# Kernel tuning notes

Hardware: AMD Instinct MI355X
Metric: run time of the kernel (lower is better)

Reference implementation:

```python
import jax, jax.numpy as jnp
import numpy as np

B, LQ, LKV, LT, C, H = 4, 1024, 1344, 320, 768, 12
DH = C // H
SCALE = DH ** -0.5
HID = 4 * C
EPS = 1e-5


def _ln(x, g, b):
    m = jnp.mean(x, axis=-1, keepdims=True)
    v = jnp.mean((x - m) ** 2, axis=-1, keepdims=True)
    return (x - m) * jax.lax.rsqrt(v + EPS) * g + b


def setup_inputs() -> dict:
    key = jax.random.key(0)
    ks = jax.random.split(key, 16)
    s = lambda k, shape, sc=0.02: jax.random.normal(k, shape, dtype=jnp.float32) * sc
    return {
        "tem_mask": s(ks[0], (B, LT, C), 1.0),
        "q": s(ks[1], (B, LQ, C), 1.0),
        "kv": s(ks[2], (B, LKV, C), 1.0),
        "attn_pos": s(ks[3], (1, H, LQ, LKV), 1.0),
        "ln1q_g": jnp.ones((C,)), "ln1q_b": jnp.zeros((C,)),
        "ln1kv_g": jnp.ones((C,)), "ln1kv_b": jnp.zeros((C,)),
        "Wq": s(ks[4], (C, C)), "bq": jnp.zeros((C,)),
        "Wkv": s(ks[5], (C, 2 * C)), "bkv": jnp.zeros((2 * C,)),
        "Wp": s(ks[6], (C, C)), "bp": jnp.zeros((C,)),
        "ln2_g": jnp.ones((C,)), "ln2_b": jnp.zeros((C,)),
        "W1": s(ks[7], (C, HID)), "b1": jnp.zeros((HID,)),
        "W2": s(ks[8], (HID, C)), "b2": jnp.zeros((C,)),
    }


def reference(tem_mask, q, kv, attn_pos, ln1q_g, ln1q_b, ln1kv_g, ln1kv_b,
              Wq, bq, Wkv, bkv, Wp, bp, ln2_g, ln2_b, W1, b1, W2, b2):
    qn = _ln(q, ln1q_g, ln1q_b)
    kvn = _ln(kv, ln1kv_g, ln1kv_b)
    # projections (attn_pos_encoding_only branch)
    qh = (qn @ Wq + bq).reshape(B, LQ, H, DH).transpose(0, 2, 1, 3)  # (B,H,Lq,Dh)
    kvp = kvn @ Wkv + bkv
    k, v = kvp[:, :, :C], kvp[:, :, C:]
    v = v.at[:, :LT, :].add(tem_mask)  # add template mask to template tokens
    kh = k.reshape(B, LKV, H, DH).transpose(0, 2, 1, 3)
    vh = v.reshape(B, LKV, H, DH).transpose(0, 2, 1, 3)
    attn = jnp.einsum('bhqd,bhkd->bhqk', qh, kh) * SCALE + attn_pos
    attn = jax.nn.softmax(attn, axis=-1)
    x = jnp.einsum('bhqk,bhkd->bhqd', attn, vh)
    x = x.transpose(0, 2, 1, 3).reshape(B, LQ, C)
    x = x @ Wp + bp
    q = q + x  # residual 1 (drop_path = Identity, dropout eval)
    h = _ln(q, ln2_g, ln2_b)
    h = jax.nn.gelu(h @ W1 + b1, approximate=False)
    h = h @ W2 + b2
    return q + h
```

## Files before the change

kernel.cpp:

```cpp
#include <hip/hip_runtime.h>
#include <hip/hip_bf16.h>
#include <math.h>

typedef __bf16 bf16x8 __attribute__((ext_vector_type(8)));
typedef float f32x4 __attribute__((ext_vector_type(4)));

__device__ __forceinline__ __hip_bfloat16 f2bf(float v){ return __float2bfloat16(v); }

__device__ __forceinline__ void gload16(const void* g, void* l){
  __builtin_amdgcn_global_load_lds(
      (const __attribute__((address_space(1))) void*)g,
      (__attribute__((address_space(3))) void*)l, 16, 0, 0);
}

__device__ __forceinline__ void ln_body(const float* rp, const float* g, const float* b,
                                        __hip_bfloat16* op, int t){
  float x0 = rp[t], x1 = rp[t+256], x2 = rp[t+512];
  float s = x0+x1+x2, ss = x0*x0+x1*x1+x2*x2;
#pragma unroll
  for(int o=32;o>0;o>>=1){ s += __shfl_down(s,o); ss += __shfl_down(ss,o); }
  __shared__ float red[10];
  if((t&63)==0){ red[t>>6]=s; red[4+(t>>6)]=ss; }
  __syncthreads();
  if(t==0){
    float S=red[0]+red[1]+red[2]+red[3], SS=red[4]+red[5]+red[6]+red[7];
    float m=S*(1.f/768.f);
    red[8]=m; red[9]=SS*(1.f/768.f)-m*m;
  }
  __syncthreads();
  float m=red[8], r=rsqrtf(red[9]+1e-5f);
  op[t]     = f2bf((x0-m)*r*g[t]     + b[t]);
  op[t+256] = f2bf((x1-m)*r*g[t+256] + b[t+256]);
  op[t+512] = f2bf((x2-m)*r*g[t+512] + b[t+512]);
}

__global__ __launch_bounds__(256) void prep_kernel(
    const float* __restrict__ Wq, const float* __restrict__ Wkv,
    const float* __restrict__ Wp, const float* __restrict__ W1,
    const float* __restrict__ W2,
    __hip_bfloat16* __restrict__ oq, __hip_bfloat16* __restrict__ okv,
    __hip_bfloat16* __restrict__ op_, __hip_bfloat16* __restrict__ o1,
    __hip_bfloat16* __restrict__ o2,
    const float* __restrict__ q, const float* __restrict__ kv,
    const float* __restrict__ qg, const float* __restrict__ qb,
    const float* __restrict__ kg, const float* __restrict__ kb2,
    __hip_bfloat16* __restrict__ qn, __hip_bfloat16* __restrict__ kvn){
  const int bid = blockIdx.x;
  const int tid = threadIdx.x;
  if(bid < 6912){
    __shared__ float tile[32][33];
    const float* in; __hip_bfloat16* out; int K, N, local;
    if(bid < 576)        { in=Wq;  out=oq;  K=768;  N=768;  local=bid; }
    else if(bid < 1728)  { in=Wkv; out=okv; K=768;  N=1536; local=bid-576; }
    else if(bid < 2304)  { in=Wp;  out=op_; K=768;  N=768;  local=bid-1728; }
    else if(bid < 4608)  { in=W1;  out=o1;  K=768;  N=3072; local=bid-2304; }
    else                 { in=W2;  out=o2;  K=3072; N=768;  local=bid-4608; }
    const int nbx = N/32;
    const int n0 = (local % nbx)*32, k0 = (local / nbx)*32;
    const int tx = tid & 31, ty = tid >> 5;
#pragma unroll
    for(int i=0;i<4;i++) tile[ty+i*8][tx] = in[(size_t)(k0+ty+i*8)*N + n0+tx];
    __syncthreads();
#pragma unroll
    for(int i=0;i<4;i++) out[(size_t)(n0+ty+i*8)*K + k0+tx] = f2bf(tile[tx][ty+i*8]);
  } else {
    int row = bid - 6912;
    if(row < 4096) ln_body(q + (size_t)row*768, qg, qb, qn + (size_t)row*768, tid);
    else { row -= 4096; ln_body(kv + (size_t)row*768, kg, kb2, kvn + (size_t)row*768, tid); }
  }
}

__global__ __launch_bounds__(256) void ln_kernel(const float* __restrict__ in,
    const float* __restrict__ g, const float* __restrict__ b,
    __hip_bfloat16* __restrict__ out){
  int row = blockIdx.x, t = threadIdx.x;
  ln_body(in + (size_t)row*768, g, b, out + (size_t)row*768, t);
}

template<int BM, int BN, int EPI>
__global__ __launch_bounds__(256) void gemm_gl(
    const __hip_bfloat16* __restrict__ A, const __hip_bfloat16* __restrict__ BT,
    const float* __restrict__ bias, int M, int N, int K,
    void* __restrict__ out, const void* __restrict__ aux0, void* __restrict__ out2){
  constexpr int WR = (BM==128 || BN==64) ? 2 : 1;
  constexpr int WC = 4/WR;
  constexpr int MF = BM/(WR*16);
  constexpr int NF = BN/(WC*16);
  constexpr int NBUF = (BM==64 && BN==64) ? 3 : 2;
  constexpr int LPS = BM/32 + BN/32;
  __shared__ char sA[NBUF][BM*128];
  __shared__ char sB[NBUF][BN*128];
  const int tid = threadIdx.x;
  const int l = tid & 63, w = tid >> 6;
  const int lg = l >> 4, li = l & 15;
  const int wrow = (WR==2) ? (w>>1)*(BM/2) : 0;
  const int wcol = (WC==2) ? (w&1)*(BN/2) : w*(BN/4);
  const int bm = blockIdx.x * BM;
  const int bn = blockIdx.y * BN;
  const int arow = w*(BM/4) + (l>>3);
  const int brow = w*(BN/4) + (l>>3);
  const int scol = ((((l&7)*16) ^ ((l>>3)<<4)) >> 1);

  auto stage = [&](int buf, int kt){
    const int k0 = kt*64;
#pragma unroll
    for(int i=0;i<BM/32;i++)
      gload16(A  + (size_t)(bm+arow+i*8)*K + k0 + scol, sA[buf] + (w*(BM/4))*128 + i*1024);
#pragma unroll
    for(int i=0;i<BN/32;i++)
      gload16(BT + (size_t)(bn+brow+i*8)*K + k0 + scol, sB[buf] + (w*(BN/4))*128 + i*1024);
  };

  f32x4 acc[MF][NF] = {};
  const int nk = K >> 6;

  if constexpr(NBUF==3){
    stage(0, 0);
    stage(1, 1);
  } else {
    stage(0, 0);
    __syncthreads();
  }

  for(int kt=0; kt<nk; ++kt){
    const char *cA, *cB;
    if constexpr(NBUF==3){
      if(kt+1 < nk) asm volatile("s_waitcnt vmcnt(%0)" :: "i"(LPS) : "memory");
      else          asm volatile("s_waitcnt vmcnt(0)" ::: "memory");
      __builtin_amdgcn_s_barrier();
      if(kt+2 < nk) stage((kt+2)%3, kt+2);
      cA = sA[kt%3]; cB = sB[kt%3];
    } else {
      const int cur = kt & 1;
      if(kt+1 < nk) stage(cur^1, kt+1);
      cA = sA[cur]; cB = sB[cur];
    }
#pragma unroll
    for(int kk=0;kk<2;kk++){
      const int kb = kk*64 + lg*16;
      bf16x8 af[MF], bfr[NF];
#pragma unroll
      for(int m=0;m<MF;m++){
        int row = wrow+m*16+li;
        af[m] = *(const bf16x8*)(cA + row*128 + (kb ^ ((row&7)<<4)));
      }
#pragma unroll
      for(int n=0;n<NF;n++){
        int row = wcol+n*16+li;
        bfr[n] = *(const bf16x8*)(cB + row*128 + (kb ^ ((row&7)<<4)));
      }
#pragma unroll
      for(int m=0;m<MF;m++)
#pragma unroll
        for(int n=0;n<NF;n++)
          acc[m][n] = __builtin_amdgcn_mfma_f32_16x16x32_bf16(af[m], bfr[n], acc[m][n],0,0,0);
    }
    if constexpr(NBUF==2) __syncthreads();
  }
#pragma unroll
  for(int m=0;m<MF;m++){
#pragma unroll
    for(int n=0;n<NF;n++){
      if constexpr(EPI==1){
        const int col = bn + wcol + n*16 + li;
        const int row0 = bm + wrow + m*16 + lg*4;
        const int bb = row0 / 1344, ii = row0 % 1344;
        if(col < 768){
#pragma unroll
          for(int r=0;r<4;r++)
            ((__hip_bfloat16*)out)[(size_t)(row0+r)*768 + col] = f2bf(acc[m][n][r] + bias[col]);
        } else {
          const int c = col - 768, hh = c >> 6, d = c & 63;
          __hip_bfloat16 tmp[4];
#pragma unroll
          for(int r=0;r<4;r++){
            float v = acc[m][n][r] + bias[col];
            if(ii < 320) v += ((const float*)aux0)[((size_t)bb*320 + ii + r)*768 + c];
            tmp[r] = f2bf(v);
          }
          *(uint2*)((__hip_bfloat16*)out2 + ((size_t)(bb*12+hh)*64 + d)*1344 + ii) = *(const uint2*)tmp;
        }
      } else {
#pragma unroll
        for(int r=0;r<4;r++){
          int row = bm + wrow + m*16 + lg*4 + r;
          int col = bn + wcol + n*16 + li;
          float v = acc[m][n][r] + bias[col];
          if constexpr(EPI==0){
            ((__hip_bfloat16*)out)[(size_t)row*N + col] = f2bf(v * 0.125f);
          } else if constexpr(EPI==2){
            v += ((const float*)aux0)[(size_t)row*N + col];
            ((float*)out)[(size_t)row*N + col] = v;
          } else if constexpr(EPI==3){
            float u = v*(0.7978845608f + 0.0356774081f*v*v);
            float e = __expf(-2.f*fabsf(u));
            float th = (1.f - e)/(1.f + e);
            th = (u < 0.f) ? -th : th;
            ((__hip_bfloat16*)out)[(size_t)row*N + col] = f2bf(0.5f*v*(1.f+th));
          } else {
            v += ((const float*)aux0)[(size_t)row*N + col];
            ((float*)out)[(size_t)row*N + col] = v;
          }
        }
      }
    }
  }
}

__global__ __launch_bounds__(256) void attn_kernel(
    const __hip_bfloat16* __restrict__ qh,
    const __hip_bfloat16* __restrict__ kb,
    const __hip_bfloat16* __restrict__ vt,
    const float* __restrict__ pos,
    __hip_bfloat16* __restrict__ xo){
  __shared__ char sK[2][8192];
  __shared__ char sV[2][8192];
  __shared__ char sP[4][2048];
  const int bid = blockIdx.x;
  const int qt = bid & 15, h = (bid >> 4) % 12, b = bid / 192;
  const int q0 = qt * 64;
  const int tid = threadIdx.x;
  const int l = tid & 63, w = tid >> 6;
  const int lg = l >> 4, li = l & 15;

  const int srow = w*16 + (l>>3);
  const int soff = (((l&7)*16) ^ ((l>>3)<<4)) >> 1;
  const __hip_bfloat16* ksrc = kb + ((size_t)b*1344 + srow)*768 + h*64 + soff;
  const __hip_bfloat16* vsrc = vt + ((size_t)(b*12+h)*64 + srow)*1344 + soff;

  bf16x8 aq[2];
  {
    const char* qp = (const char*)(qh + ((size_t)(b*1024 + q0 + w*16 + li))*768 + h*64);
    aq[0] = *(const bf16x8*)(qp + lg*16);
    aq[1] = *(const bf16x8*)(qp + 64 + lg*16);
  }
  bf16x8 ones;
#pragma unroll
  for(int i=0;i<8;i++) ones[i] = (__bf16)1.0f;
  const size_t posbase = ((size_t)h*1024 + q0 + w*16 + lg*4)*1344 + li;

  f32x4 accO[4] = {};
  f32x4 accL = {};
  float mrun[4];
#pragma unroll
  for(int r=0;r<4;r++) mrun[r] = -1e30f;

  auto stage = [&](int buf, int t){
    const size_t ko = (size_t)t*64*768;
    const size_t vo = (size_t)t*64;
    gload16(ksrc + ko,          sK[buf] + w*2048);
    gload16(ksrc + ko + 8*768,  sK[buf] + w*2048 + 1024);
    gload16(vsrc + vo,          sV[buf] + w*2048);
    gload16(vsrc + vo + 8*1344, sV[buf] + w*2048 + 1024);
  };
  auto ldpos = [&](int t, float (&pr)[4][4]){
    const float* pp = pos + posbase + (size_t)t*64;
#pragma unroll
    for(int n=0;n<4;n++)
#pragma unroll
      for(int r=0;r<4;r++)
        pr[n][r] = __builtin_nontemporal_load(pp + (size_t)r*1344 + n*16);
  };

  float pA[4][4], pB[4][4];
  ldpos(0, pA);
  stage(0, 0);
  __syncthreads();

  char* sPw = sP[w];

  auto body = [&](int t, float (&posr)[4][4], float (&npos)[4][4]){
    const int cur = t & 1;
    const bool more = (t < 20);
    f32x4 accS[4] = {};
    __builtin_amdgcn_s_setprio(1);
#pragma unroll
    for(int kk=0; kk<2; ++kk){
      const int kbyte = kk*64 + lg*16;
#pragma unroll
      for(int n=0;n<4;n++){
        int row = n*16 + li;
        bf16x8 bkf = *(const bf16x8*)(sK[cur] + row*128 + (kbyte ^ ((row&7)<<4)));
        accS[n] = __builtin_amdgcn_mfma_f32_16x16x32_bf16(aq[kk], bkf, accS[n], 0,0,0);
      }
    }
    __builtin_amdgcn_s_setprio(0);
    if(more) stage(cur^1, t+1);
    asm volatile("" ::: "memory");
    if(more) ldpos(t+1, npos);

    float p[4][4], mt[4];
#pragma unroll
    for(int r=0;r<4;r++) mt[r] = -1e30f;
#pragma unroll
    for(int n=0;n<4;n++)
#pragma unroll
      for(int r=0;r<4;r++){
        float s = accS[n][r] + posr[n][r];
        p[n][r] = s;
        mt[r] = fmaxf(mt[r], s);
      }
    bool need = false;
#pragma unroll
    for(int r=0;r<4;r++) need |= (mt[r] > mrun[r] + 8.f);
    if(__any(need)){
#pragma unroll
      for(int r=0;r<4;r++){
#pragma unroll
        for(int o=1;o<16;o<<=1) mt[r] = fmaxf(mt[r], __shfl_xor(mt[r], o));
        float mnew = fmaxf(mrun[r], mt[r]);
        float sf = __expf(mrun[r]-mnew);
        mrun[r] = mnew;
        accL[r] *= sf;
#pragma unroll
        for(int n=0;n<4;n++) accO[n][r] *= sf;
      }
    }
#pragma unroll
    for(int n=0;n<4;n++)
#pragma unroll
      for(int r=0;r<4;r++) p[n][r] = __expf(p[n][r]-mrun[r]);
#pragma unroll
    for(int n=0;n<4;n++)
#pragma unroll
      for(int r=0;r<4;r++){
        int qi = lg*4 + r, kj = n*16 + li;
        *(__hip_bfloat16*)(sPw + qi*128 + ((kj*2) ^ ((qi&7)<<4))) = f2bf(p[n][r]);
      }
    __builtin_amdgcn_s_setprio(1);
#pragma unroll
    for(int kk=0; kk<2; ++kk){
      const int kbyte = kk*64 + lg*16;
      bf16x8 pa = *(const bf16x8*)(sPw + li*128 + (kbyte ^ ((li&7)<<4)));
      accL = __builtin_amdgcn_mfma_f32_16x16x32_bf16(pa, ones, accL, 0,0,0);
#pragma unroll
      for(int n=0;n<4;n++){
        int d = n*16 + li;
        bf16x8 bvf = *(const bf16x8*)(sV[cur] + d*128 + (kbyte ^ ((d&7)<<4)));
        accO[n] = __builtin_amdgcn_mfma_f32_16x16x32_bf16(pa, bvf, accO[n], 0,0,0);
      }
    }
    __builtin_amdgcn_s_setprio(0);
    if(more){
      asm volatile("s_waitcnt vmcnt(16)" ::: "memory");
      __builtin_amdgcn_s_barrier();
    }
  };

  for(int tt=0; tt<10; ++tt){
    body(2*tt,   pA, pB);
    body(2*tt+1, pB, pA);
  }
  body(20, pA, pB);

#pragma unroll
  for(int n=0;n<4;n++)
#pragma unroll
    for(int r=0;r<4;r++){
      int row = b*1024 + q0 + w*16 + lg*4 + r;
      int col = h*64 + n*16 + li;
      xo[(size_t)row*768 + col] = f2bf(accO[n][r] / accL[r]);
    }
}

extern "C" void kernel_launch(void* const* d_in, const int* in_sizes, int n_in,
                              void* d_out, int out_size, void* d_ws, size_t ws_size,
                              hipStream_t stream){
  const float* tem   = (const float*)d_in[0];
  const float* qin   = (const float*)d_in[1];
  const float* kvin  = (const float*)d_in[2];
  const float* pos   = (const float*)d_in[3];
  const float* ln1qg = (const float*)d_in[4];
  const float* ln1qb = (const float*)d_in[5];
  const float* ln1kg = (const float*)d_in[6];
  const float* ln1kb = (const float*)d_in[7];
  const float* Wq    = (const float*)d_in[8];
  const float* bq    = (const float*)d_in[9];
  const float* Wkv   = (const float*)d_in[10];
  const float* bkv   = (const float*)d_in[11];
  const float* Wp    = (const float*)d_in[12];
  const float* bp    = (const float*)d_in[13];
  const float* ln2g  = (const float*)d_in[14];
  const float* ln2b  = (const float*)d_in[15];
  const float* W1    = (const float*)d_in[16];
  const float* b1    = (const float*)d_in[17];
  const float* W2    = (const float*)d_in[18];
  const float* b2    = (const float*)d_in[19];

  char* ws = (char*)d_ws; size_t off = 0;
  auto alloc = [&](size_t n){ char* p = ws + off; off = (off + n + 255) & ~(size_t)255; return p; };
  __hip_bfloat16* WqT  = (__hip_bfloat16*)alloc((size_t)768*768*2);
  __hip_bfloat16* WkvT = (__hip_bfloat16*)alloc((size_t)1536*768*2);
  __hip_bfloat16* WpT  = (__hip_bfloat16*)alloc((size_t)768*768*2);
  __hip_bfloat16* W1T  = (__hip_bfloat16*)alloc((size_t)3072*768*2);
  __hip_bfloat16* W2T  = (__hip_bfloat16*)alloc((size_t)768*3072*2);
  __hip_bfloat16* qn   = (__hip_bfloat16*)alloc((size_t)4096*768*2);
  char* poolBase = alloc((size_t)5376*768*2*3 + (size_t)4096*768*2);
  __hip_bfloat16* kvn  = (__hip_bfloat16*)poolBase;
  __hip_bfloat16* kbuf = kvn  + (size_t)5376*768;
  __hip_bfloat16* vt   = kbuf + (size_t)5376*768;
  __hip_bfloat16* qhb  = vt   + (size_t)5376*768;
  __hip_bfloat16* xat  = (__hip_bfloat16*)alloc((size_t)4096*768*2);
  float*          x1f  = (float*)alloc((size_t)4096*768*4);
  __hip_bfloat16* hln  = qn;
  __hip_bfloat16* h1   = kvn;

  prep_kernel<<<16384, 256, 0, stream>>>(Wq, Wkv, Wp, W1, W2, WqT, WkvT, WpT, W1T, W2T,
                                         qin, kvin, ln1qg, ln1qb, ln1kg, ln1kb, qn, kvn);

  gemm_gl<64,64,0>  <<<dim3(64, 12), 256, 0, stream>>>(qn,  WqT,  bq,  4096, 768,  768,  qhb, nullptr, nullptr);
  gemm_gl<128,128,1><<<dim3(42, 12), 256, 0, stream>>>(kvn, WkvT, bkv, 5376, 1536, 768,  kbuf, tem, vt);

  attn_kernel<<<768, 256, 0, stream>>>(qhb, kbuf, vt, pos, xat);

  gemm_gl<64,64,2>  <<<dim3(64, 12), 256, 0, stream>>>(xat, WpT,  bp,  4096, 768,  768,  x1f, qin, nullptr);
  ln_kernel<<<4096, 256, 0, stream>>>(x1f, ln2g, ln2b, hln);
  gemm_gl<128,128,3><<<dim3(32, 24), 256, 0, stream>>>(hln, W1T,  b1,  4096, 3072, 768,  h1, nullptr, nullptr);
  gemm_gl<64,64,4>  <<<dim3(64, 12), 256, 0, stream>>>(h1,  W2T,  b2,  4096, 768,  3072, (float*)d_out, x1f, nullptr);
}
```

Measured before the change: 221.0 us.

## Compute transposed QK^T so each lane owns one query row in flash attention

Swaps the MFMA operands so the score tile comes out transposed, which gives each lane a single query row with 16 contiguous key columns. The running max becomes one scalar per lane and needs only two cross-lane shuffles instead of sixteen. The attn_pos bias is now read as four 16-byte vector loads per tile instead of sixteen scalar loads, and P is written to LDS as 8-byte packed stores. The rescale factor is redistributed with shuffles to match the output accumulator layout, and the vmcnt wait threshold is changed to match the smaller number of outstanding loads.

```diff
diff --git a/kernel.cpp b/kernel.cpp
--- a/kernel.cpp
+++ b/kernel.cpp
@@ -237,13 +237,11 @@
   bf16x8 ones;
 #pragma unroll
   for(int i=0;i<8;i++) ones[i] = (__bf16)1.0f;
-  const size_t posbase = ((size_t)h*1024 + q0 + w*16 + lg*4)*1344 + li;
+  const size_t posbase = ((size_t)h*1024 + q0 + w*16 + li)*1344 + lg*4;
 
   f32x4 accO[4] = {};
   f32x4 accL = {};
-  float mrun[4];
-#pragma unroll
-  for(int r=0;r<4;r++) mrun[r] = -1e30f;
+  float mrun = -1e30f;
 
   auto stage = [&](int buf, int t){
     const size_t ko = (size_t)t*64*768;
@@ -253,35 +251,33 @@
     gload16(vsrc + vo,          sV[buf] + w*2048);
     gload16(vsrc + vo + 8*1344, sV[buf] + w*2048 + 1024);
   };
-  auto ldpos = [&](int t, float (&pr)[4][4]){
+  auto ldpos = [&](int t, f32x4 (&pr)[4]){
     const float* pp = pos + posbase + (size_t)t*64;
 #pragma unroll
-    for(int n=0;n<4;n++)
-#pragma unroll
-      for(int r=0;r<4;r++)
-        pr[n][r] = __builtin_nontemporal_load(pp + (size_t)r*1344 + n*16);
+    for(int m=0;m<4;m++)
+      pr[m] = __builtin_nontemporal_load((const f32x4*)(pp + m*16));
   };
 
-  float pA[4][4], pB[4][4];
+  f32x4 pA[4], pB[4];
   ldpos(0, pA);
   stage(0, 0);
   __syncthreads();
 
   char* sPw = sP[w];
 
-  auto body = [&](int t, float (&posr)[4][4], float (&npos)[4][4]){
+  auto body = [&](int t, f32x4 (&posr)[4], f32x4 (&npos)[4]){
     const int cur = t & 1;
     const bool more = (t < 20);
-    f32x4 accS[4] = {};
+    f32x4 accT[4] = {};
     __builtin_amdgcn_s_setprio(1);
 #pragma unroll
     for(int kk=0; kk<2; ++kk){
       const int kbyte = kk*64 + lg*16;
 #pragma unroll
-      for(int n=0;n<4;n++){
-        int row = n*16 + li;
+      for(int m=0;m<4;m++){
+        int row = m*16 + li;
         bf16x8 bkf = *(const bf16x8*)(sK[cur] + row*128 + (kbyte ^ ((row&7)<<4)));
-        accS[n] = __builtin_amdgcn_mfma_f32_16x16x32_bf16(aq[kk], bkf, accS[n], 0,0,0);
+        accT[m] = __builtin_amdgcn_mfma_f32_16x16x32_bf16(bkf, aq[kk], accT[m], 0,0,0);
       }
     }
     __builtin_amdgcn_s_setprio(0);
@@ -289,44 +285,43 @@
     asm volatile("" ::: "memory");
     if(more) ldpos(t+1, npos);
 
-    float p[4][4], mt[4];
-#pragma unroll
-    for(int r=0;r<4;r++) mt[r] = -1e30f;
-#pragma unroll
-    for(int n=0;n<4;n++)
+    float p[4][4];
+    float mt = -1e30f;
+#pragma unroll
+    for(int m=0;m<4;m++)
 #pragma unroll
       for(int r=0;r<4;r++){
-        float s = accS[n][r] + posr[n][r];
-        p[n][r] = s;
-        mt[r] = fmaxf(mt[r], s);
-      }
-    bool need = false;
-#pragma unroll
-    for(int r=0;r<4;r++) need |= (mt[r] > mrun[r] + 8.f);
-    if(__any(need)){
+        float s = accT[m][r] + posr[m][r];
+        p[m][r] = s;
+        mt = fmaxf(mt, s);
+      }
+    if(__any(mt > mrun + 8.f)){
+      float mf = mt;
+      mf = fmaxf(mf, __shfl_xor(mf, 16));
+      mf = fmaxf(mf, __shfl_xor(mf, 32));
+      float mnew = fmaxf(mrun, mf);
+      float sf = __expf(mrun - mnew);
+      mrun = mnew;
 #pragma unroll
       for(int r=0;r<4;r++){
-#pragma unroll
-        for(int o=1;o<16;o<<=1) mt[r] = fmaxf(mt[r], __shfl_xor(mt[r], o));
-        float mnew = fmaxf(mrun[r], mt[r]);
-        float sf = __expf(mrun[r]-mnew);
-        mrun[r] = mnew;
-        accL[r] *= sf;
-#pragma unroll
-        for(int n=0;n<4;n++) accO[n][r] *= sf;
-      }
-    }
-#pragma unroll
-    for(int n=0;n<4;n++)
-#pragma unroll
-      for(int r=0;r<4;r++) p[n][r] = __expf(p[n][r]-mrun[r]);
-#pragma unroll
-    for(int n=0;n<4;n++)
-#pragma unroll
-      for(int r=0;r<4;r++){
-        int qi = lg*4 + r, kj = n*16 + li;
-        *(__hip_bfloat16*)(sPw + qi*128 + ((kj*2) ^ ((qi&7)<<4))) = f2bf(p[n][r]);
-      }
+        float sfr = __shfl(sf, lg*4 + r);
+        accL[r] *= sfr;
+#pragma unroll
+        for(int n=0;n<4;n++) accO[n][r] *= sfr;
+      }
+    }
+#pragma unroll
+    for(int m=0;m<4;m++)
+#pragma unroll
+      for(int r=0;r<4;r++) p[m][r] = __expf(p[m][r]-mrun);
+#pragma unroll
+    for(int m=0;m<4;m++){
+      __hip_bfloat16 t4[4];
+#pragma unroll
+      for(int r=0;r<4;r++) t4[r] = f2bf(p[m][r]);
+      const int off = (m*32 + lg*8) ^ ((li&7)<<4);
+      *(uint2*)(sPw + li*128 + off) = *(const uint2*)t4;
+    }
     __builtin_amdgcn_s_setprio(1);
 #pragma unroll
     for(int kk=0; kk<2; ++kk){
@@ -342,7 +337,7 @@
     }
     __builtin_amdgcn_s_setprio(0);
     if(more){
-      asm volatile("s_waitcnt vmcnt(16)" ::: "memory");
+      asm volatile("s_waitcnt vmcnt(4)" ::: "memory");
       __builtin_amdgcn_s_barrier();
     }
   };
```

Result: no change. 225.2 us (+1.9%).
